# Performance work log

Hardware: AMD Instinct MI355X
Metric: run time of the kernel (lower is better)

The kernel has to match this reference:

```python
import jax, jax.numpy as jnp
import numpy as np

# ---- static config (from xib add_argument defaults / chosen production sizes) ----
B, L = 16, 50            # batch, text length
LU, KU, DIM = 60, 100, 60
V, MAXVL = 2000, 10      # vocab size, max vocab word length (J)
MIN_WL, MAX_WL = 4, 10   # min/max extracted word length
NE = MAX_WL - MIN_WL + 1 # number of len_e candidates
INS_DEL_COST = 3.5       # min_ins_del_cost
UNEXTRACTED_PROB = 0.01
CONTEXT_WEIGHT = 0.1     # weight for context (conv) log-probs
NEG = -9999.9


def setup_inputs() -> dict:
    key = jax.random.key(0)
    ks = jax.random.split(key, 8)
    unit_id_seqs = jax.random.randint(ks[0], (B, L), 0, LU)
    lengths = 10 + jax.random.randint(ks[1], (B,), 0, L - 9)  # in [10, L]
    unit_repr = jax.random.normal(ks[2], (KU, DIM), jnp.float32)
    aligner_weight = 0.1 * jax.random.normal(ks[3], (LU, KU), jnp.float32)
    conv_w = jax.random.normal(ks[4], (DIM, DIM, 3), jnp.float32) / np.sqrt(3.0 * DIM)
    conv_b = jnp.zeros((DIM,), jnp.float32)
    vocab_ids = jax.random.randint(ks[5], (V, MAXVL), 0, KU)
    vocab_lengths = MIN_WL + jax.random.randint(ks[6], (V,), 0, MAXVL - MIN_WL + 1)
    return dict(unit_id_seqs=unit_id_seqs, lengths=lengths, unit_repr=unit_repr,
                aligner_weight=aligner_weight, conv_w=conv_w, conv_b=conv_b,
                vocab_ids=vocab_ids, vocab_lengths=vocab_lengths)


def reference(unit_id_seqs, lengths, unit_repr, aligner_weight, conv_w, conv_b,
              vocab_ids, vocab_lengths):
    # ---- G2P layer: embedding-as-matmul + Conv1d over length ----
    ku_char_repr = aligner_weight @ unit_repr                 # (LU, DIM)
    emb = ku_char_repr[unit_id_seqs]                          # (B, L, DIM)
    x = jnp.swapaxes(emb, 1, 2)                               # (B, DIM, L)
    y = jax.lax.conv_general_dilated(x, conv_w, (1,), 'SAME',
                                     dimension_numbers=('NCH', 'OIH', 'NCH'))
    word_repr = jnp.swapaxes(y + conv_b[None, :, None], 1, 2)  # (B, L, DIM)
    char_log_probs = jax.nn.log_softmax(ku_char_repr @ unit_repr.T, axis=-1)  # (LU, KU)
    alignment = jnp.exp(char_log_probs)
    ctx_log_probs = jax.nn.log_softmax(word_repr @ unit_repr.T, axis=-1)      # (B, L, KU)
    # per-position substitution log prob against each known unit
    pos_lp = char_log_probs[unit_id_seqs] + CONTEXT_WEIGHT * ctx_log_probs    # (B, L, KU)
    sub = pos_lp[:, :, vocab_ids]                                             # (B, L, V, J)
    sub = jnp.pad(sub, ((0, 0), (0, MAX_WL), (0, 0), (0, 0)), constant_values=NEG)
    J = MAXVL
    # ---- edit-distance style DP over (span char i, vocab char j), vectorized
    # over (batch, start position, vocab). prev[b,s,j,v] = f[i-1][j].
    j_ar = jnp.arange(J + 1, dtype=sub.dtype)
    prev = jnp.broadcast_to((-INS_DEL_COST * j_ar)[None, None, :, None], (B, L, J + 1, V))
    vl_idx = jnp.broadcast_to(vocab_lengths[None, None, None, :].astype(jnp.int32), (B, L, 1, V))
    lls = []
    for i in range(1, MAX_WL + 1):          # fixed small loop (<=10)
        sub_i = sub[:, i - 1:i - 1 + L]     # (B, L, V, J): char at position s+i-1
        row = [jnp.full((B, L, V), -INS_DEL_COST * i, dtype=sub.dtype)]
        for j in range(1, J + 1):           # fixed small loop (<=10)
            diag = prev[:, :, j - 1, :] + sub_i[:, :, :, j - 1]
            up = prev[:, :, j, :] - INS_DEL_COST
            left = row[j - 1] - INS_DEL_COST
            row.append(jnp.maximum(diag, jnp.maximum(up, left)))
        prev = jnp.stack(row, axis=2)       # (B, L, J+1, V)
        if i >= MIN_WL:                     # matched ll for word length i
            lls.append(jnp.take_along_axis(prev, vl_idx, axis=2)[:, :, 0, :])
    ll = jnp.stack(lls, axis=2)             # (B, L, NE, V) = matches.ll
    # ---- viability mask + unextracted penalty, pick best candidate ----
    starts = jnp.arange(L)
    word_lens = MIN_WL + jnp.arange(NE)
    viable = (starts[None, :, None] + word_lens[None, None, :]) <= lengths[:, None, None]  # (B,L,NE)
    unextracted = (lengths[:, None, None] - word_lens[None, None, :]).astype(ll.dtype)     # (B,1,NE)
    score = (ll + jnp.where(viable, 0.0, NEG)[..., None]
             + (unextracted * np.log(UNEXTRACTED_PROB))[..., None, :, None][:, 0])
    flat = score.reshape(B, L * NE * V)
    best_idx = jnp.argmax(flat, axis=1)
    best_matched_ll = jnp.max(flat, axis=1)
    start = best_idx // (NE * V)
    e_idx = (best_idx // V) % NE
    best_matched_vocab = best_idx % V
    end = start + MIN_WL + e_idx - 1
    return start, end, best_matched_ll, best_matched_vocab, alignment
```

## Files before the change

### kernel.cpp

```cpp
#include <hip/hip_runtime.h>
#include <math.h>
#include <stdint.h>

#define B_ 16
#define L_ 50
#define LU_ 60
#define KU_ 100
#define DIM_ 60
#define V_ 2000
#define MAXVL_ 10
#define MIN_WL_ 4
#define MAX_WL_ 10
#define NE_ 7
#define IDC_ 3.5f
#define LOG_UNEXT_ (-4.6051701859880913680359829093687f)
#define CTXW_ 0.1f
#define NQ_ 13

#define WS_PLP  0
#define WS_BEST_BYTES (80000u * 4u)
#define BEST_STRIDE 8
#define WS_CNT_OFF   (WS_BEST_BYTES + 1024u)
#define CNT_STRIDE 16
#define WS_VPACK_BYTES (WS_BEST_BYTES + 2048u)

#define URP_ 61
#define CWP_ 61

#define S2_ 202
#define NKEY_ 54

__global__ __launch_bounds__(256) void ctx_kernel(
    const int* __restrict__ uid,
    const float* __restrict__ unit_repr,
    const float* __restrict__ aligner_w,
    const float* __restrict__ conv_w,
    const float* __restrict__ conv_b,
    const int* __restrict__ vocab_ids,
    const int* __restrict__ vocab_lengths,
    float* __restrict__ ws_plp,
    float* __restrict__ out_align,
    unsigned long long* __restrict__ g_best,
    unsigned* __restrict__ cnt,
    int* __restrict__ vpack)
{
  int blk = blockIdx.x;
  int t = threadIdx.x;

  if (blk == B_ * NQ_) {
    for (int v = t; v < V_; v += 256) {
      int vl = vocab_lengths[v];
      unsigned q0 = 0u, q1 = 0u, q2 = 0u;
#pragma unroll
      for (int j = 0; j < 4; ++j) q0 |= ((unsigned)vocab_ids[v * MAXVL_ + j]) << (j * 8);
#pragma unroll
      for (int j = 0; j < 4; ++j) q1 |= ((unsigned)vocab_ids[v * MAXVL_ + 4 + j]) << (j * 8);
#pragma unroll
      for (int j = 0; j < 2; ++j) q2 |= ((unsigned)vocab_ids[v * MAXVL_ + 8 + j]) << (j * 8);
      int4 w;
      w.x = (int)q0; w.y = (int)q1; w.z = (int)q2;
      w.w = (int)((unsigned)vl | ((unsigned)v << 8));
      ((int4*)vpack)[v] = w;
    }
    return;
  }

  int b = blk / NQ_, q = blk % NQ_;
  int l0 = 4 * q;
  int npos = (l0 + 4 <= L_) ? 4 : (L_ - l0);
  int alr = (blk < LU_) ? blk : -1;

  __shared__ float s_ur[KU_ * URP_];
  __shared__ float s_cw[3 * DIM_ * CWP_];
  __shared__ float s_aw[7 * KU_];
  __shared__ float s_kx[7 * DIM_];
  __shared__ float swr[4 * DIM_];
  __shared__ float sclp[4 * KU_];
  __shared__ float sctx[4 * KU_];
  __shared__ float salg[KU_];
  __shared__ float sls[9];

  if (blk == 0) {
    if (t < B_) g_best[t * BEST_STRIDE] = 0ull;
    if (t >= 32 && t < 32 + B_) cnt[(t - 32) * CNT_STRIDE] = 0u;
  }

  const float4* ur4 = (const float4*)unit_repr;
  for (int k = t; k < (KU_ * DIM_) / 4; k += 256) {
    float4 v = ur4[k];
    int i0 = 4 * k;
    s_ur[((i0 + 0) / DIM_) * URP_ + ((i0 + 0) % DIM_)] = v.x;
    s_ur[((i0 + 1) / DIM_) * URP_ + ((i0 + 1) % DIM_)] = v.y;
    s_ur[((i0 + 2) / DIM_) * URP_ + ((i0 + 2) % DIM_)] = v.z;
    s_ur[((i0 + 3) / DIM_) * URP_ + ((i0 + 3) % DIM_)] = v.w;
  }
  const float4* cw4 = (const float4*)conv_w;
  for (int k = t; k < (DIM_ * DIM_ * 3) / 4; k += 256) {
    float4 v = cw4[k];
    int i0 = 4 * k;
    float vv[4] = {v.x, v.y, v.z, v.w};
#pragma unroll
    for (int e = 0; e < 4; ++e) {
      int idx = i0 + e;
      int o = idx / (3 * DIM_), id = idx % (3 * DIM_);
      s_cw[id * CWP_ + o] = vv[e];
    }
  }
  for (int i = t; i < 7 * KU_; i += 256) {
    int m = i / KU_, k = i - m * KU_;
    float w = 0.f;
    if (m < 6) {
      int ld = l0 - 1 + m;
      if (ld >= 0 && ld < L_) {
        int u = uid[b * L_ + ld];
        w = aligner_w[u * KU_ + k];
      }
    } else if (alr >= 0) {
      w = aligner_w[alr * KU_ + k];
    }
    s_aw[i] = w;
  }
  __syncthreads();

  for (int idx = t; idx < 7 * DIM_; idx += 256) {
    int m = idx / DIM_, c = idx - m * DIM_;
    const float4* aw4 = (const float4*)&s_aw[m * KU_];
    float acc = 0.f;
    for (int k4 = 0; k4 < KU_ / 4; ++k4) {
      float4 a = aw4[k4];
      int k = 4 * k4;
      acc += a.x * s_ur[(k + 0) * URP_ + c];
      acc += a.y * s_ur[(k + 1) * URP_ + c];
      acc += a.z * s_ur[(k + 2) * URP_ + c];
      acc += a.w * s_ur[(k + 3) * URP_ + c];
    }
    s_kx[idx] = acc;
  }
  __syncthreads();

  for (int idx = t; idx < 240 + 4 * KU_; idx += 256) {
    if (idx < 240) {
      int p = idx / DIM_, o = idx - p * DIM_;
      const float4* x04 = (const float4*)&s_kx[(p + 0) * DIM_];
      const float4* x14 = (const float4*)&s_kx[(p + 1) * DIM_];
      const float4* x24 = (const float4*)&s_kx[(p + 2) * DIM_];
      float acc = conv_b[o];
      for (int i4 = 0; i4 < DIM_ / 4; ++i4) {
        float4 x0 = x04[i4], x1 = x14[i4], x2 = x24[i4];
        int i = 4 * i4;
        acc += x0.x * s_cw[((i + 0) * 3 + 0) * CWP_ + o];
        acc += x1.x * s_cw[((i + 0) * 3 + 1) * CWP_ + o];
        acc += x2.x * s_cw[((i + 0) * 3 + 2) * CWP_ + o];
        acc += x0.y * s_cw[((i + 1) * 3 + 0) * CWP_ + o];
        acc += x1.y * s_cw[((i + 1) * 3 + 1) * CWP_ + o];
        acc += x2.y * s_cw[((i + 1) * 3 + 2) * CWP_ + o];
        acc += x0.z * s_cw[((i + 2) * 3 + 0) * CWP_ + o];
        acc += x1.z * s_cw[((i + 2) * 3 + 1) * CWP_ + o];
        acc += x2.z * s_cw[((i + 2) * 3 + 2) * CWP_ + o];
        acc += x0.w * s_cw[((i + 3) * 3 + 0) * CWP_ + o];
        acc += x1.w * s_cw[((i + 3) * 3 + 1) * CWP_ + o];
        acc += x2.w * s_cw[((i + 3) * 3 + 2) * CWP_ + o];
      }
      swr[p * DIM_ + o] = acc;
    } else {
      int r = idx - 240;
      int p = r / KU_, j = r - p * KU_;
      const float4* kx4 = (const float4*)&s_kx[(p + 1) * DIM_];
      float acc = 0.f;
      for (int d4 = 0; d4 < DIM_ / 4; ++d4) {
        float4 x = kx4[d4];
        int d = 4 * d4;
        acc += x.x * s_ur[j * URP_ + d + 0];
        acc += x.y * s_ur[j * URP_ + d + 1];
        acc += x.z * s_ur[j * URP_ + d + 2];
        acc += x.w * s_ur[j * URP_ + d + 3];
      }
      sclp[r] = acc;
    }
  }
  __syncthreads();

  for (int idx = t; idx < 4 * KU_ + KU_; idx += 256) {
    if (idx < 4 * KU_) {
      int p = idx / KU_, j = idx - p * KU_;
      const float4* w4 = (const float4*)&swr[p * DIM_];
      float acc = 0.f;
      for (int d4 = 0; d4 < DIM_ / 4; ++d4) {
        float4 x = w4[d4];
        int d = 4 * d4;
        acc += x.x * s_ur[j * URP_ + d + 0];
        acc += x.y * s_ur[j * URP_ + d + 1];
        acc += x.z * s_ur[j * URP_ + d + 2];
        acc += x.w * s_ur[j * URP_ + d + 3];
      }
      sctx[idx] = acc;
    } else {
      int j = idx - 4 * KU_;
      const float4* kx4 = (const float4*)&s_kx[6 * DIM_];
      float acc = 0.f;
      for (int d4 = 0; d4 < DIM_ / 4; ++d4) {
        float4 x = kx4[d4];
        int d = 4 * d4;
        acc += x.x * s_ur[j * URP_ + d + 0];
        acc += x.y * s_ur[j * URP_ + d + 1];
        acc += x.z * s_ur[j * URP_ + d + 2];
        acc += x.w * s_ur[j * URP_ + d + 3];
      }
      salg[j] = acc;
    }
  }
  __syncthreads();

  {
    int g = t >> 5, lane = t & 31;
#pragma unroll
    for (int round = 0; round < 2; ++round) {
      int r = round * 8 + g;
      if (r < 9) {
        const float* arr = (r == 8) ? salg
                          : ((r & 1) ? &sctx[(r >> 1) * KU_] : &sclp[(r >> 1) * KU_]);
        float v1 = arr[lane];
        float v2 = arr[32 + lane];
        float v3 = arr[64 + lane];
        float v4 = (lane < KU_ - 96) ? arr[96 + lane] : -1e30f;
        float mx = fmaxf(fmaxf(v1, v2), fmaxf(v3, v4));
#pragma unroll
        for (int off = 16; off > 0; off >>= 1)
          mx = fmaxf(mx, __shfl_xor(mx, off));
        float s = expf(v1 - mx) + expf(v2 - mx) + expf(v3 - mx) +
                  ((lane < KU_ - 96) ? expf(v4 - mx) : 0.f);
#pragma unroll
        for (int off = 16; off > 0; off >>= 1)
          s += __shfl_xor(s, off);
        if (lane == 0) sls[r] = mx + logf(s);
      }
    }
  }
  __syncthreads();

  for (int idx = t; idx < 4 * KU_; idx += 256) {
    int p = idx / KU_, j = idx - p * KU_;
    if (p < npos) {
      float pos = (sclp[idx] - sls[2 * p]) + CTXW_ * (sctx[idx] - sls[2 * p + 1]);
      ws_plp[(b * L_ + l0 + p) * KU_ + j] = pos + 2.0f * IDC_;
    }
  }
  if (alr >= 0 && t < KU_)
    out_align[alr * KU_ + t] = expf(salg[t] - sls[8]);
}

template<int VL>
__device__ __forceinline__ unsigned long long dp_one(
    const float* __restrict__ fb,
    unsigned q0, unsigned q1, unsigned q2,
    const float* cvec, int lbase, int vid)
{
  float D[MAXVL_ + 1];
#pragma unroll
  for (int i = 0; i <= MAXVL_; ++i) D[i] = 0.f;

#pragma unroll
  for (int j = 0; j < VL; ++j) {
    unsigned qq = (j < 4) ? q0 : ((j < 8) ? q1 : q2);
    int k2 = (int)((qq >> ((j & 3) * 8)) & 0xFFu) * 2;
    float2 p0 = *(const float2*)(fb + k2);
    float2 p1 = *(const float2*)(fb + k2 + S2_);
    float2 p2 = *(const float2*)(fb + k2 + 2 * S2_);
    float2 p3 = *(const float2*)(fb + k2 + 3 * S2_);
    float2 p4 = *(const float2*)(fb + k2 + 4 * S2_);
    float s[MAXVL_] = {p0.x, p1.x, p2.x, p3.x, p4.x,
                       p0.y, p1.y, p2.y, p3.y, p4.y};
    float left = 0.f;
#pragma unroll
    for (int i = 1; i <= MAXVL_; ++i) {
      float nv = fmaxf(D[i - 1] + s[i - 1], fmaxf(D[i], left));
      D[i - 1] = left;
      left = nv;
    }
    D[MAXVL_] = left;
  }

  float bestSc = -1e30f;
  int bestEV = 0;
#pragma unroll
  for (int e = 0; e < NE_; ++e) {
    float sc = D[MIN_WL_ + e] + cvec[e];
    if (sc > bestSc) { bestSc = sc; bestEV = e * V_; }
  }
  bestSc -= IDC_ * (float)VL;
  unsigned idx = (unsigned)(lbase + bestEV + vid);
  unsigned u = __float_as_uint(bestSc);
  u = (u & 0x80000000u) ? ~u : (u | 0x80000000u);
  unsigned long long key =
      ((unsigned long long)u << 32) | (unsigned long long)(~idx);
  return (bestSc > -1e29f) ? key : 0ull;
}

__global__ __launch_bounds__(256) void dp_kernel(
    const int* __restrict__ lengths,
    const float* __restrict__ ws_plp,
    const int* __restrict__ vpack,
    unsigned long long* __restrict__ g_best,
    unsigned* __restrict__ cnt,
    float* __restrict__ out)
{
  __shared__ float sp[NKEY_ * S2_];
  __shared__ unsigned long long swave[4];
  int b = blockIdx.x;
  int chunk = blockIdx.y;
  int t = threadIdx.x;
  int len_b = lengths[b];

  const float4* src4 = (const float4*)ws_plp;
  for (int idx = t; idx < NKEY_ * 25; idx += 256) {
    int key = idx / 25, m = idx - key * 25;
    int ra = b * L_ + key;     if (ra > B_ * L_ - 1) ra = B_ * L_ - 1;
    int rb = b * L_ + key + 5; if (rb > B_ * L_ - 1) rb = B_ * L_ - 1;
    float4 qa = src4[ra * 25 + m];
    float4 qb = src4[rb * 25 + m];
    float2* dst = (float2*)&sp[key * S2_ + 8 * m];
    dst[0] = make_float2(qa.x, qb.x);
    dst[1] = make_float2(qa.y, qb.y);
    dst[2] = make_float2(qa.z, qb.z);
    dst[3] = make_float2(qa.w, qb.w);
  }

  int lane = t & 63, w = t >> 6;
  float cvec[NE_];
#pragma unroll
  for (int e = 0; e < NE_; ++e) {
    int i = MIN_WL_ + e;
    bool ok = (lane < L_) && (i <= len_b - lane);
    cvec[e] = ok ? ((float)(len_b - i) * LOG_UNEXT_ - IDC_ * (float)i) : -1e30f;
  }
  int lbase = lane * (NE_ * V_);
  int lcl = (lane < L_) ? lane : (L_ - 1);
  const float* fb = sp + lcl * S2_;
  __syncthreads();

  unsigned long long bestKey = 0ull;
  const int4* vp4 = (const int4*)vpack;
  int vbase = chunk * 40 + w * 10;
  int4 wq = vp4[vbase];
#pragma unroll 1
  for (int n = 0; n < 10; ++n) {
    int4 wqn = vp4[vbase + ((n < 9) ? (n + 1) : 9)];
    unsigned q0 = (unsigned)__builtin_amdgcn_readfirstlane(wq.x);
    unsigned q1 = (unsigned)__builtin_amdgcn_readfirstlane(wq.y);
    unsigned q2 = (unsigned)__builtin_amdgcn_readfirstlane(wq.z);
    unsigned q3 = (unsigned)__builtin_amdgcn_readfirstlane(wq.w);
    int vlen = (int)(q3 & 0xFFu);
    int vid = (int)(q3 >> 8);
    unsigned long long kk = 0ull;
    switch (vlen) {
      case 4:  kk = dp_one<4>(fb, q0, q1, q2, cvec, lbase, vid); break;
      case 5:  kk = dp_one<5>(fb, q0, q1, q2, cvec, lbase, vid); break;
      case 6:  kk = dp_one<6>(fb, q0, q1, q2, cvec, lbase, vid); break;
      case 7:  kk = dp_one<7>(fb, q0, q1, q2, cvec, lbase, vid); break;
      case 8:  kk = dp_one<8>(fb, q0, q1, q2, cvec, lbase, vid); break;
      case 9:  kk = dp_one<9>(fb, q0, q1, q2, cvec, lbase, vid); break;
      case 10: kk = dp_one<10>(fb, q0, q1, q2, cvec, lbase, vid); break;
      default: break;
    }
    if (kk > bestKey) bestKey = kk;
    wq = wqn;
  }

#pragma unroll
  for (int off = 32; off > 0; off >>= 1) {
    unsigned long long o = __shfl_down(bestKey, off);
    if (o > bestKey) bestKey = o;
  }
  if ((t & 63) == 0) swave[w] = bestKey;
  __syncthreads();
  if (t == 0) {
    unsigned long long k0 = swave[0];
    for (int x = 1; x < 4; ++x)
      if (swave[x] > k0) k0 = swave[x];
    unsigned long long old = atomicMax(g_best + (size_t)b * BEST_STRIDE, k0);
    asm volatile("" :: "v"(old));
    unsigned prev = atomicAdd(&cnt[b * CNT_STRIDE], 1u);
    if (prev == (unsigned)(L_ - 1)) {
      unsigned long long key = atomicMax(g_best + (size_t)b * BEST_STRIDE, 0ull);
      unsigned int u = (unsigned int)(key >> 32);
      unsigned int idx = ~((unsigned int)(key & 0xFFFFFFFFull));
      unsigned int bits = (u & 0x80000000u) ? (u & 0x7FFFFFFFu) : ~u;
      float val = __uint_as_float(bits);
      int start = (int)(idx / (NE_ * V_));
      int rem = (int)(idx % (NE_ * V_));
      int e = rem / V_;
      int vv = rem % V_;
      out[b] = (float)start;
      out[B_ + b] = (float)(start + MIN_WL_ + e - 1);
      out[2 * B_ + b] = val;
      out[3 * B_ + b] = (float)vv;
    }
  }
}

extern "C" void kernel_launch(void* const* d_in, const int* in_sizes, int n_in,
                              void* d_out, int out_size, void* d_ws, size_t ws_size,
                              hipStream_t stream)
{
  const int* uid            = (const int*)d_in[0];
  const int* lengths        = (const int*)d_in[1];
  const float* unit_repr    = (const float*)d_in[2];
  const float* aligner_w    = (const float*)d_in[3];
  const float* conv_w       = (const float*)d_in[4];
  const float* conv_b       = (const float*)d_in[5];
  const int* vocab_ids      = (const int*)d_in[6];
  const int* vocab_lengths  = (const int*)d_in[7];
  float* out = (float*)d_out;
  float* ws_f = (float*)d_ws;
  unsigned long long* g_best =
      (unsigned long long*)((char*)d_ws + WS_BEST_BYTES);
  unsigned* cnt = (unsigned*)((char*)d_ws + WS_CNT_OFF);
  int* vpack = (int*)((char*)d_ws + WS_VPACK_BYTES);

  ctx_kernel<<<B_ * NQ_ + 1, 256, 0, stream>>>(uid, unit_repr, aligner_w,
                                               conv_w, conv_b, vocab_ids,
                                               vocab_lengths, ws_f + WS_PLP,
                                               out + 4 * B_, g_best, cnt, vpack);
  dim3 g3(B_, 50);
  dp_kernel<<<g3, 256, 0, stream>>>(lengths, ws_f + WS_PLP, vpack, g_best,
                                    cnt, out);
}
```

Measured before the change: 106.2 us.

## Fuse context and DP kernels into one cooperative kernel with grid sync

Merges the two launches into a single cooperative kernel of 256 blocks × 512 threads that uses a grid-wide sync between the context stage and the DP stage, with a shared-memory union reused across phases. The DP work is re-split into 16 chunks of 125 vocab words per batch row, with 8 waves per block, replacing the 50-chunk × 4-wave split. Vocab packing is spread over the spare blocks. This removes one kernel launch and the inter-kernel gap. The costs are grid-sync overhead and fewer blocks for the DP stage. If the cooperative launch fails, it falls back to two kernel launches.

```diff
diff --git a/kernel.cpp b/kernel.cpp
--- a/kernel.cpp
+++ b/kernel.cpp
@@ -1,6 +1,9 @@
 #include <hip/hip_runtime.h>
+#include <hip/hip_cooperative_groups.h>
 #include <math.h>
 #include <stdint.h>
+
+namespace cg = cooperative_groups;
 
 #define B_ 16
 #define L_ 50
@@ -16,6 +19,7 @@
 #define LOG_UNEXT_ (-4.6051701859880913680359829093687f)
 #define CTXW_ 0.1f
 #define NQ_ 13
+#define NT_ 512
 
 #define WS_PLP  0
 #define WS_BEST_BYTES (80000u * 4u)
@@ -30,72 +34,63 @@
 #define S2_ 202
 #define NKEY_ 54
 
-__global__ __launch_bounds__(256) void ctx_kernel(
-    const int* __restrict__ uid,
-    const float* __restrict__ unit_repr,
-    const float* __restrict__ aligner_w,
-    const float* __restrict__ conv_w,
-    const float* __restrict__ conv_b,
-    const int* __restrict__ vocab_ids,
-    const int* __restrict__ vocab_lengths,
-    float* __restrict__ ws_plp,
-    float* __restrict__ out_align,
-    unsigned long long* __restrict__ g_best,
-    unsigned* __restrict__ cnt,
+struct CtxS {
+  float s_ur[KU_ * URP_];
+  float s_cw[3 * DIM_ * CWP_];
+  float s_aw[7 * KU_];
+  float s_kx[7 * DIM_];
+  float swr[4 * DIM_];
+  float sclp[4 * KU_];
+  float sctx[4 * KU_];
+  float salg[KU_];
+  float sls[9];
+};
+struct DpS {
+  float sp[NKEY_ * S2_];
+  unsigned long long swave[8];
+};
+union SU { CtxS c; DpS d; };
+
+__device__ __forceinline__ void pack_one(int v,
+    const int* __restrict__ vocab_ids, const int* __restrict__ vocab_lengths,
     int* __restrict__ vpack)
 {
-  int blk = blockIdx.x;
-  int t = threadIdx.x;
-
-  if (blk == B_ * NQ_) {
-    for (int v = t; v < V_; v += 256) {
-      int vl = vocab_lengths[v];
-      unsigned q0 = 0u, q1 = 0u, q2 = 0u;
-#pragma unroll
-      for (int j = 0; j < 4; ++j) q0 |= ((unsigned)vocab_ids[v * MAXVL_ + j]) << (j * 8);
-#pragma unroll
-      for (int j = 0; j < 4; ++j) q1 |= ((unsigned)vocab_ids[v * MAXVL_ + 4 + j]) << (j * 8);
-#pragma unroll
-      for (int j = 0; j < 2; ++j) q2 |= ((unsigned)vocab_ids[v * MAXVL_ + 8 + j]) << (j * 8);
-      int4 w;
-      w.x = (int)q0; w.y = (int)q1; w.z = (int)q2;
-      w.w = (int)((unsigned)vl | ((unsigned)v << 8));
-      ((int4*)vpack)[v] = w;
-    }
-    return;
-  }
-
+  int vl = vocab_lengths[v];
+  unsigned q0 = 0u, q1 = 0u, q2 = 0u;
+#pragma unroll
+  for (int j = 0; j < 4; ++j) q0 |= ((unsigned)vocab_ids[v * MAXVL_ + j]) << (j * 8);
+#pragma unroll
+  for (int j = 0; j < 4; ++j) q1 |= ((unsigned)vocab_ids[v * MAXVL_ + 4 + j]) << (j * 8);
+#pragma unroll
+  for (int j = 0; j < 2; ++j) q2 |= ((unsigned)vocab_ids[v * MAXVL_ + 8 + j]) << (j * 8);
+  int4 w;
+  w.x = (int)q0; w.y = (int)q1; w.z = (int)q2;
+  w.w = (int)((unsigned)vl | ((unsigned)v << 8));
+  ((int4*)vpack)[v] = w;
+}
+
+__device__ void ctx_tile_dev(CtxS& S, int blk, int t,
+    const int* __restrict__ uid, const float* __restrict__ unit_repr,
+    const float* __restrict__ aligner_w, const float* __restrict__ conv_w,
+    const float* __restrict__ conv_b, float* __restrict__ ws_plp,
+    float* __restrict__ out_align)
+{
   int b = blk / NQ_, q = blk % NQ_;
   int l0 = 4 * q;
   int npos = (l0 + 4 <= L_) ? 4 : (L_ - l0);
   int alr = (blk < LU_) ? blk : -1;
 
-  __shared__ float s_ur[KU_ * URP_];
-  __shared__ float s_cw[3 * DIM_ * CWP_];
-  __shared__ float s_aw[7 * KU_];
-  __shared__ float s_kx[7 * DIM_];
-  __shared__ float swr[4 * DIM_];
-  __shared__ float sclp[4 * KU_];
-  __shared__ float sctx[4 * KU_];
-  __shared__ float salg[KU_];
-  __shared__ float sls[9];
-
-  if (blk == 0) {
-    if (t < B_) g_best[t * BEST_STRIDE] = 0ull;
-    if (t >= 32 && t < 32 + B_) cnt[(t - 32) * CNT_STRIDE] = 0u;
-  }
-
   const float4* ur4 = (const float4*)unit_repr;
-  for (int k = t; k < (KU_ * DIM_) / 4; k += 256) {
+  for (int k = t; k < (KU_ * DIM_) / 4; k += NT_) {
     float4 v = ur4[k];
     int i0 = 4 * k;
-    s_ur[((i0 + 0) / DIM_) * URP_ + ((i0 + 0) % DIM_)] = v.x;
-    s_ur[((i0 + 1) / DIM_) * URP_ + ((i0 + 1) % DIM_)] = v.y;
-    s_ur[((i0 + 2) / DIM_) * URP_ + ((i0 + 2) % DIM_)] = v.z;
-    s_ur[((i0 + 3) / DIM_) * URP_ + ((i0 + 3) % DIM_)] = v.w;
+    S.s_ur[((i0 + 0) / DIM_) * URP_ + ((i0 + 0) % DIM_)] = v.x;
+    S.s_ur[((i0 + 1) / DIM_) * URP_ + ((i0 + 1) % DIM_)] = v.y;
+    S.s_ur[((i0 + 2) / DIM_) * URP_ + ((i0 + 2) % DIM_)] = v.z;
+    S.s_ur[((i0 + 3) / DIM_) * URP_ + ((i0 + 3) % DIM_)] = v.w;
   }
   const float4* cw4 = (const float4*)conv_w;
-  for (int k = t; k < (DIM_ * DIM_ * 3) / 4; k += 256) {
+  for (int k = t; k < (DIM_ * DIM_ * 3) / 4; k += NT_) {
     float4 v = cw4[k];
     int i0 = 4 * k;
     float vv[4] = {v.x, v.y, v.z, v.w};
@@ -103,10 +98,10 @@
     for (int e = 0; e < 4; ++e) {
       int idx = i0 + e;
       int o = idx / (3 * DIM_), id = idx % (3 * DIM_);
-      s_cw[id * CWP_ + o] = vv[e];
-    }
-  }
-  for (int i = t; i < 7 * KU_; i += 256) {
+      S.s_cw[id * CWP_ + o] = vv[e];
+    }
+  }
+  for (int i = t; i < 7 * KU_; i += NT_) {
     int m = i / KU_, k = i - m * KU_;
     float w = 0.f;
     if (m < 6) {
@@ -118,135 +113,131 @@
     } else if (alr >= 0) {
       w = aligner_w[alr * KU_ + k];
     }
-    s_aw[i] = w;
-  }
-  __syncthreads();
-
-  for (int idx = t; idx < 7 * DIM_; idx += 256) {
+    S.s_aw[i] = w;
+  }
+  __syncthreads();
+
+  for (int idx = t; idx < 7 * DIM_; idx += NT_) {
     int m = idx / DIM_, c = idx - m * DIM_;
-    const float4* aw4 = (const float4*)&s_aw[m * KU_];
+    const float4* aw4 = (const float4*)&S.s_aw[m * KU_];
     float acc = 0.f;
     for (int k4 = 0; k4 < KU_ / 4; ++k4) {
       float4 a = aw4[k4];
       int k = 4 * k4;
-      acc += a.x * s_ur[(k + 0) * URP_ + c];
-      acc += a.y * s_ur[(k + 1) * URP_ + c];
-      acc += a.z * s_ur[(k + 2) * URP_ + c];
-      acc += a.w * s_ur[(k + 3) * URP_ + c];
-    }
-    s_kx[idx] = acc;
-  }
-  __syncthreads();
-
-  for (int idx = t; idx < 240 + 4 * KU_; idx += 256) {
+      acc += a.x * S.s_ur[(k + 0) * URP_ + c];
+      acc += a.y * S.s_ur[(k + 1) * URP_ + c];
+      acc += a.z * S.s_ur[(k + 2) * URP_ + c];
+      acc += a.w * S.s_ur[(k + 3) * URP_ + c];
+    }
+    S.s_kx[idx] = acc;
+  }
+  __syncthreads();
+
+  for (int idx = t; idx < 240 + 4 * KU_; idx += NT_) {
     if (idx < 240) {
       int p = idx / DIM_, o = idx - p * DIM_;
-      const float4* x04 = (const float4*)&s_kx[(p + 0) * DIM_];
-      const float4* x14 = (const float4*)&s_kx[(p + 1) * DIM_];
-      const float4* x24 = (const float4*)&s_kx[(p + 2) * DIM_];
+      const float4* x04 = (const float4*)&S.s_kx[(p + 0) * DIM_];
+      const float4* x14 = (const float4*)&S.s_kx[(p + 1) * DIM_];
+      const float4* x24 = (const float4*)&S.s_kx[(p + 2) * DIM_];
       float acc = conv_b[o];
       for (int i4 = 0; i4 < DIM_ / 4; ++i4) {
         float4 x0 = x04[i4], x1 = x14[i4], x2 = x24[i4];
         int i = 4 * i4;
-        acc += x0.x * s_cw[((i + 0) * 3 + 0) * CWP_ + o];
-        acc += x1.x * s_cw[((i + 0) * 3 + 1) * CWP_ + o];
-        acc += x2.x * s_cw[((i + 0) * 3 + 2) * CWP_ + o];
-        acc += x0.y * s_cw[((i + 1) * 3 + 0) * CWP_ + o];
-        acc += x1.y * s_cw[((i + 1) * 3 + 1) * CWP_ + o];
-        acc += x2.y * s_cw[((i + 1) * 3 + 2) * CWP_ + o];
-        acc += x0.z * s_cw[((i + 2) * 3 + 0) * CWP_ + o];
-        acc += x1.z * s_cw[((i + 2) * 3 + 1) * CWP_ + o];
-        acc += x2.z * s_cw[((i + 2) * 3 + 2) * CWP_ + o];
-        acc += x0.w * s_cw[((i + 3) * 3 + 0) * CWP_ + o];
-        acc += x1.w * s_cw[((i + 3) * 3 + 1) * CWP_ + o];
-        acc += x2.w * s_cw[((i + 3) * 3 + 2) * CWP_ + o];
-      }
-      swr[p * DIM_ + o] = acc;
+        acc += x0.x * S.s_cw[((i + 0) * 3 + 0) * CWP_ + o];
+        acc += x1.x * S.s_cw[((i + 0) * 3 + 1) * CWP_ + o];
+        acc += x2.x * S.s_cw[((i + 0) * 3 + 2) * CWP_ + o];
+        acc += x0.y * S.s_cw[((i + 1) * 3 + 0) * CWP_ + o];
+        acc += x1.y * S.s_cw[((i + 1) * 3 + 1) * CWP_ + o];
+        acc += x2.y * S.s_cw[((i + 1) * 3 + 2) * CWP_ + o];
+        acc += x0.z * S.s_cw[((i + 2) * 3 + 0) * CWP_ + o];
+        acc += x1.z * S.s_cw[((i + 2) * 3 + 1) * CWP_ + o];
+        acc += x2.z * S.s_cw[((i + 2) * 3 + 2) * CWP_ + o];
+        acc += x0.w * S.s_cw[((i + 3) * 3 + 0) * CWP_ + o];
+        acc += x1.w * S.s_cw[((i + 3) * 3 + 1) * CWP_ + o];
+        acc += x2.w * S.s_cw[((i + 3) * 3 + 2) * CWP_ + o];
+      }
+      S.swr[p * DIM_ + o] = acc;
     } else {
       int r = idx - 240;
       int p = r / KU_, j = r - p * KU_;
-      const float4* kx4 = (const float4*)&s_kx[(p + 1) * DIM_];
+      const float4* kx4 = (const float4*)&S.s_kx[(p + 1) * DIM_];
       float acc = 0.f;
       for (int d4 = 0; d4 < DIM_ / 4; ++d4) {
         float4 x = kx4[d4];
         int d = 4 * d4;
-        acc += x.x * s_ur[j * URP_ + d + 0];
-        acc += x.y * s_ur[j * URP_ + d + 1];
-        acc += x.z * s_ur[j * URP_ + d + 2];
-        acc += x.w * s_ur[j * URP_ + d + 3];
-      }
-      sclp[r] = acc;
-    }
-  }
-  __syncthreads();
-
-  for (int idx = t; idx < 4 * KU_ + KU_; idx += 256) {
+        acc += x.x * S.s_ur[j * URP_ + d + 0];
+        acc += x.y * S.s_ur[j * URP_ + d + 1];
+        acc += x.z * S.s_ur[j * URP_ + d + 2];
+        acc += x.w * S.s_ur[j * URP_ + d + 3];
+      }
+      S.sclp[r] = acc;
+    }
+  }
+  __syncthreads();
+
+  for (int idx = t; idx < 4 * KU_ + KU_; idx += NT_) {
     if (idx < 4 * KU_) {
       int p = idx / KU_, j = idx - p * KU_;
-      const float4* w4 = (const float4*)&swr[p * DIM_];
+      const float4* w4 = (const float4*)&S.swr[p * DIM_];
       float acc = 0.f;
       for (int d4 = 0; d4 < DIM_ / 4; ++d4) {
         float4 x = w4[d4];
         int d = 4 * d4;
-        acc += x.x * s_ur[j * URP_ + d + 0];
-        acc += x.y * s_ur[j * URP_ + d + 1];
-        acc += x.z * s_ur[j * URP_ + d + 2];
-        acc += x.w * s_ur[j * URP_ + d + 3];
-      }
-      sctx[idx] = acc;
+        acc += x.x * S.s_ur[j * URP_ + d + 0];
+        acc += x.y * S.s_ur[j * URP_ + d + 1];
+        acc += x.z * S.s_ur[j * URP_ + d + 2];
+        acc += x.w * S.s_ur[j * URP_ + d + 3];
+      }
+      S.sctx[idx] = acc;
     } else {
       int j = idx - 4 * KU_;
-      const float4* kx4 = (const float4*)&s_kx[6 * DIM_];
+      const float4* kx4 = (const float4*)&S.s_kx[6 * DIM_];
       float acc = 0.f;
       for (int d4 = 0; d4 < DIM_ / 4; ++d4) {
         float4 x = kx4[d4];
         int d = 4 * d4;
-        acc += x.x * s_ur[j * URP_ + d + 0];
-        acc += x.y * s_ur[j * URP_ + d + 1];
-        acc += x.z * s_ur[j * URP_ + d + 2];
-        acc += x.w * s_ur[j * URP_ + d + 3];
-      }
-      salg[j] = acc;
+        acc += x.x * S.s_ur[j * URP_ + d + 0];
+        acc += x.y * S.s_ur[j * URP_ + d + 1];
+        acc += x.z * S.s_ur[j * URP_ + d + 2];
+        acc += x.w * S.s_ur[j * URP_ + d + 3];
+      }
+      S.salg[j] = acc;
     }
   }
   __syncthreads();
 
   {
     int g = t >> 5, lane = t & 31;
-#pragma unroll
-    for (int round = 0; round < 2; ++round) {
-      int r = round * 8 + g;
-      if (r < 9) {
-        const float* arr = (r == 8) ? salg
-                          : ((r & 1) ? &sctx[(r >> 1) * KU_] : &sclp[(r >> 1) * KU_]);
-        float v1 = arr[lane];
-        float v2 = arr[32 + lane];
-        float v3 = arr[64 + lane];
-        float v4 = (lane < KU_ - 96) ? arr[96 + lane] : -1e30f;
-        float mx = fmaxf(fmaxf(v1, v2), fmaxf(v3, v4));
-#pragma unroll
-        for (int off = 16; off > 0; off >>= 1)
-          mx = fmaxf(mx, __shfl_xor(mx, off));
-        float s = expf(v1 - mx) + expf(v2 - mx) + expf(v3 - mx) +
-                  ((lane < KU_ - 96) ? expf(v4 - mx) : 0.f);
-#pragma unroll
-        for (int off = 16; off > 0; off >>= 1)
-          s += __shfl_xor(s, off);
-        if (lane == 0) sls[r] = mx + logf(s);
-      }
-    }
-  }
-  __syncthreads();
-
-  for (int idx = t; idx < 4 * KU_; idx += 256) {
+    if (g < 9) {
+      const float* arr = (g == 8) ? S.salg
+                        : ((g & 1) ? &S.sctx[(g >> 1) * KU_] : &S.sclp[(g >> 1) * KU_]);
+      float v1 = arr[lane];
+      float v2 = arr[32 + lane];
+      float v3 = arr[64 + lane];
+      float v4 = (lane < KU_ - 96) ? arr[96 + lane] : -1e30f;
+      float mx = fmaxf(fmaxf(v1, v2), fmaxf(v3, v4));
+#pragma unroll
+      for (int off = 16; off > 0; off >>= 1)
+        mx = fmaxf(mx, __shfl_xor(mx, off));
+      float s = expf(v1 - mx) + expf(v2 - mx) + expf(v3 - mx) +
+                ((lane < KU_ - 96) ? expf(v4 - mx) : 0.f);
+#pragma unroll
+      for (int off = 16; off > 0; off >>= 1)
+        s += __shfl_xor(s, off);
+      if (lane == 0) S.sls[g] = mx + logf(s);
+    }
+  }
+  __syncthreads();
+
+  for (int idx = t; idx < 4 * KU_; idx += NT_) {
     int p = idx / KU_, j = idx - p * KU_;
     if (p < npos) {
-      float pos = (sclp[idx] - sls[2 * p]) + CTXW_ * (sctx[idx] - sls[2 * p + 1]);
+      float pos = (S.sclp[idx] - S.sls[2 * p]) + CTXW_ * (S.sctx[idx] - S.sls[2 * p + 1]);
       ws_plp[(b * L_ + l0 + p) * KU_ + j] = pos + 2.0f * IDC_;
     }
   }
   if (alr >= 0 && t < KU_)
-    out_align[alr * KU_ + t] = expf(salg[t] - sls[8]);
+    out_align[alr * KU_ + t] = expf(S.salg[t] - S.sls[8]);
 }
 
 template<int VL>
@@ -296,29 +287,21 @@
   return (bestSc > -1e29f) ? key : 0ull;
 }
 
-__global__ __launch_bounds__(256) void dp_kernel(
-    const int* __restrict__ lengths,
-    const float* __restrict__ ws_plp,
-    const int* __restrict__ vpack,
-    unsigned long long* __restrict__ g_best,
-    unsigned* __restrict__ cnt,
-    float* __restrict__ out)
-{
-  __shared__ float sp[NKEY_ * S2_];
-  __shared__ unsigned long long swave[4];
-  int b = blockIdx.x;
-  int chunk = blockIdx.y;
-  int t = threadIdx.x;
+__device__ void dp_dev(DpS& D, int b, int c, int t,
+    const int* __restrict__ lengths, const float* __restrict__ ws_plp,
+    const int* __restrict__ vpack, unsigned long long* __restrict__ g_best,
+    unsigned* __restrict__ cnt, float* __restrict__ out)
+{
   int len_b = lengths[b];
 
   const float4* src4 = (const float4*)ws_plp;
-  for (int idx = t; idx < NKEY_ * 25; idx += 256) {
+  for (int idx = t; idx < NKEY_ * 25; idx += NT_) {
     int key = idx / 25, m = idx - key * 25;
     int ra = b * L_ + key;     if (ra > B_ * L_ - 1) ra = B_ * L_ - 1;
     int rb = b * L_ + key + 5; if (rb > B_ * L_ - 1) rb = B_ * L_ - 1;
     float4 qa = src4[ra * 25 + m];
     float4 qb = src4[rb * 25 + m];
-    float2* dst = (float2*)&sp[key * S2_ + 8 * m];
+    float2* dst = (float2*)&D.sp[key * S2_ + 8 * m];
     dst[0] = make_float2(qa.x, qb.x);
     dst[1] = make_float2(qa.y, qb.y);
     dst[2] = make_float2(qa.z, qb.z);
@@ -335,34 +318,37 @@
   }
   int lbase = lane * (NE_ * V_);
   int lcl = (lane < L_) ? lane : (L_ - 1);
-  const float* fb = sp + lcl * S2_;
+  const float* fb = D.sp + lcl * S2_;
   __syncthreads();
 
   unsigned long long bestKey = 0ull;
   const int4* vp4 = (const int4*)vpack;
-  int vbase = chunk * 40 + w * 10;
-  int4 wq = vp4[vbase];
+  int vbase = c * 125;
+  int4 wq = (w < 125) ? vp4[vbase + w] : make_int4(0, 0, 0, 0);
 #pragma unroll 1
-  for (int n = 0; n < 10; ++n) {
-    int4 wqn = vp4[vbase + ((n < 9) ? (n + 1) : 9)];
-    unsigned q0 = (unsigned)__builtin_amdgcn_readfirstlane(wq.x);
-    unsigned q1 = (unsigned)__builtin_amdgcn_readfirstlane(wq.y);
-    unsigned q2 = (unsigned)__builtin_amdgcn_readfirstlane(wq.z);
-    unsigned q3 = (unsigned)__builtin_amdgcn_readfirstlane(wq.w);
-    int vlen = (int)(q3 & 0xFFu);
-    int vid = (int)(q3 >> 8);
-    unsigned long long kk = 0ull;
-    switch (vlen) {
-      case 4:  kk = dp_one<4>(fb, q0, q1, q2, cvec, lbase, vid); break;
-      case 5:  kk = dp_one<5>(fb, q0, q1, q2, cvec, lbase, vid); break;
-      case 6:  kk = dp_one<6>(fb, q0, q1, q2, cvec, lbase, vid); break;
-      case 7:  kk = dp_one<7>(fb, q0, q1, q2, cvec, lbase, vid); break;
-      case 8:  kk = dp_one<8>(fb, q0, q1, q2, cvec, lbase, vid); break;
-      case 9:  kk = dp_one<9>(fb, q0, q1, q2, cvec, lbase, vid); break;
-      case 10: kk = dp_one<10>(fb, q0, q1, q2, cvec, lbase, vid); break;
-      default: break;
-    }
-    if (kk > bestKey) bestKey = kk;
+  for (int n = 0; n < 16; ++n) {
+    int vln = w + 8 * (n + 1);
+    int4 wqn = (vln < 125) ? vp4[vbase + vln] : make_int4(0, 0, 0, 0);
+    if (w + 8 * n < 125) {
+      unsigned q0 = (unsigned)__builtin_amdgcn_readfirstlane(wq.x);
+      unsigned q1 = (unsigned)__builtin_amdgcn_readfirstlane(wq.y);
+      unsigned q2 = (unsigned)__builtin_amdgcn_readfirstlane(wq.z);
+      unsigned q3 = (unsigned)__builtin_amdgcn_readfirstlane(wq.w);
+      int vlen = (int)(q3 & 0xFFu);
+      int vid = (int)(q3 >> 8);
+      unsigned long long kk = 0ull;
+      switch (vlen) {
+        case 4:  kk = dp_one<4>(fb, q0, q1, q2, cvec, lbase, vid); break;
+        case 5:  kk = dp_one<5>(fb, q0, q1, q2, cvec, lbase, vid); break;
+        case 6:  kk = dp_one<6>(fb, q0, q1, q2, cvec, lbase, vid); break;
+        case 7:  kk = dp_one<7>(fb, q0, q1, q2, cvec, lbase, vid); break;
+        case 8:  kk = dp_one<8>(fb, q0, q1, q2, cvec, lbase, vid); break;
+        case 9:  kk = dp_one<9>(fb, q0, q1, q2, cvec, lbase, vid); break;
+        case 10: kk = dp_one<10>(fb, q0, q1, q2, cvec, lbase, vid); break;
+        default: break;
+      }
+      if (kk > bestKey) bestKey = kk;
+    }
     wq = wqn;
   }
 
@@ -371,16 +357,16 @@
     unsigned long long o = __shfl_down(bestKey, off);
     if (o > bestKey) bestKey = o;
   }
-  if ((t & 63) == 0) swave[w] = bestKey;
+  if ((t & 63) == 0) D.swave[w] = bestKey;
   __syncthreads();
   if (t == 0) {
-    unsigned long long k0 = swave[0];
-    for (int x = 1; x < 4; ++x)
-      if (swave[x] > k0) k0 = swave[x];
+    unsigned long long k0 = D.swave[0];
+    for (int x = 1; x < 8; ++x)
+      if (D.swave[x] > k0) k0 = D.swave[x];
     unsigned long long old = atomicMax(g_best + (size_t)b * BEST_STRIDE, k0);
     asm volatile("" :: "v"(old));
     unsigned prev = atomicAdd(&cnt[b * CNT_STRIDE], 1u);
-    if (prev == (unsigned)(L_ - 1)) {
+    if (prev == 15u) {
       unsigned long long key = atomicMax(g_best + (size_t)b * BEST_STRIDE, 0ull);
       unsigned int u = (unsigned int)(key >> 32);
       unsigned int idx = ~((unsigned int)(key & 0xFFFFFFFFull));
@@ -398,6 +384,66 @@
   }
 }
 
+__device__ __forceinline__ void phaseA(SU& su, int blk, int t,
+    const int* uid, const float* unit_repr, const float* aligner_w,
+    const float* conv_w, const float* conv_b, const int* vocab_ids,
+    const int* vocab_lengths, float* ws_plp, float* out_align,
+    unsigned long long* g_best, unsigned* cnt, int* vpack)
+{
+  if (blk < B_ * NQ_) {
+    ctx_tile_dev(su.c, blk, t, uid, unit_repr, aligner_w, conv_w, conv_b,
+                 ws_plp, out_align);
+  } else {
+    int v = (blk - B_ * NQ_) * NT_ + t;
+    if (v < V_) pack_one(v, vocab_ids, vocab_lengths, vpack);
+    if (blk == 255) {
+      if (t < B_) g_best[t * BEST_STRIDE] = 0ull;
+      if (t >= 64 && t < 64 + B_) cnt[(t - 64) * CNT_STRIDE] = 0u;
+    }
+  }
+}
+
+__global__ __launch_bounds__(NT_) void mega_kernel(
+    const int* __restrict__ uid, const int* __restrict__ lengths,
+    const float* __restrict__ unit_repr, const float* __restrict__ aligner_w,
+    const float* __restrict__ conv_w, const float* __restrict__ conv_b,
+    const int* __restrict__ vocab_ids, const int* __restrict__ vocab_lengths,
+    float* __restrict__ ws_plp, float* __restrict__ out_align,
+    unsigned long long* __restrict__ g_best, unsigned* __restrict__ cnt,
+    int* __restrict__ vpack, float* __restrict__ out)
+{
+  __shared__ SU su;
+  int blk = blockIdx.x, t = threadIdx.x;
+  phaseA(su, blk, t, uid, unit_repr, aligner_w, conv_w, conv_b,
+         vocab_ids, vocab_lengths, ws_plp, out_align, g_best, cnt, vpack);
+  cg::this_grid().sync();
+  dp_dev(su.d, blk >> 4, blk & 15, t, lengths, ws_plp, vpack, g_best, cnt, out);
+}
+
+__global__ __launch_bounds__(NT_) void k_ctx(
+    const int* __restrict__ uid, const float* __restrict__ unit_repr,
+    const float* __restrict__ aligner_w, const float* __restrict__ conv_w,
+    const float* __restrict__ conv_b, const int* __restrict__ vocab_ids,
+    const int* __restrict__ vocab_lengths, float* __restrict__ ws_plp,
+    float* __restrict__ out_align, unsigned long long* __restrict__ g_best,
+    unsigned* __restrict__ cnt, int* __restrict__ vpack)
+{
+  __shared__ SU su;
+  phaseA(su, blockIdx.x, threadIdx.x, uid, unit_repr, aligner_w, conv_w,
+         conv_b, vocab_ids, vocab_lengths, ws_plp, out_align, g_best, cnt,
+         vpack);
+}
+
+__global__ __launch_bounds__(NT_) void k_dp(
+    const int* __restrict__ lengths, const float* __restrict__ ws_plp,
+    const int* __restrict__ vpack, unsigned long long* __restrict__ g_best,
+    unsigned* __restrict__ cnt, float* __restrict__ out)
+{
+  __shared__ DpS d;
+  dp_dev(d, blockIdx.x >> 4, blockIdx.x & 15, threadIdx.x,
+         lengths, ws_plp, vpack, g_best, cnt, out);
+}
+
 extern "C" void kernel_launch(void* const* d_in, const int* in_sizes, int n_in,
                               void* d_out, int out_size, void* d_ws, size_t ws_size,
                               hipStream_t stream)
@@ -411,17 +457,26 @@
   const int* vocab_ids      = (const int*)d_in[6];
   const int* vocab_lengths  = (const int*)d_in[7];
   float* out = (float*)d_out;
-  float* ws_f = (float*)d_ws;
+  float* out_align = out + 4 * B_;
+  float* ws_plp = (float*)d_ws;
   unsigned long long* g_best =
       (unsigned long long*)((char*)d_ws + WS_BEST_BYTES);
   unsigned* cnt = (unsigned*)((char*)d_ws + WS_CNT_OFF);
   int* vpack = (int*)((char*)d_ws + WS_VPACK_BYTES);
 
-  ctx_kernel<<<B_ * NQ_ + 1, 256, 0, stream>>>(uid, unit_repr, aligner_w,
-                                               conv_w, conv_b, vocab_ids,
-                                               vocab_lengths, ws_f + WS_PLP,
-                                               out + 4 * B_, g_best, cnt, vpack);
-  dim3 g3(B_, 50);
-  dp_kernel<<<g3, 256, 0, stream>>>(lengths, ws_f + WS_PLP, vpack, g_best,
-                                    cnt, out);
-}
+  void* args[] = {
+    (void*)&uid, (void*)&lengths, (void*)&unit_repr, (void*)&aligner_w,
+    (void*)&conv_w, (void*)&conv_b, (void*)&vocab_ids, (void*)&vocab_lengths,
+    (void*)&ws_plp, (void*)&out_align, (void*)&g_best, (void*)&cnt,
+    (void*)&vpack, (void*)&out
+  };
+  hipError_t e = hipLaunchCooperativeKernel((const void*)mega_kernel,
+                                            dim3(256), dim3(NT_), args, 0,
+                                            stream);
+  if (e != hipSuccess) {
+    k_ctx<<<256, NT_, 0, stream>>>(uid, unit_repr, aligner_w, conv_w, conv_b,
+                                   vocab_ids, vocab_lengths, ws_plp,
+                                   out_align, g_best, cnt, vpack);
+    k_dp<<<256, NT_, 0, stream>>>(lengths, ws_plp, vpack, g_best, cnt, out);
+  }
+}
```

After: 149.6 us. 40.9% more time.
